# Performance work log

Hardware: AMD Instinct MI355X
Metric: run time of the kernel (lower is better)

## Reference

```python
import jax, jax.numpy as jnp
import numpy as np
import math

B, CIN, COUT, K, R = 8, 128, 128, 7, 2
GC = 16                     # group_channels (init arg `groups`)
G = COUT // GC              # number of dynamic-weight groups = 8
H = W = 32
EPS = 1e-5


def c4_lift(w):
    # w: [o, i, 4] -> dense 1x1 weight [o*4, i*4] via cyclic C4 shifts
    # torch: weight[:, r] = w[..., roll-by-r]  (e.g. r=1 -> [3,0,1,2])
    Wr = jnp.stack([jnp.roll(w, r, axis=-1) for r in range(4)], axis=1)  # [o,4,i,4]
    o, _, i, _ = Wr.shape
    return Wr.reshape(o * 4, i * 4)


def setup_inputs() -> dict:
    key = jax.random.key(0)
    ks = jax.random.split(key, 4)
    sc = 1.0 / math.sqrt(4 * CIN / 2)
    x = jax.random.normal(ks[0], (B, CIN * 4, H, W), dtype=jnp.float32)
    v_w = jax.random.normal(ks[1], (COUT, CIN, 4), dtype=jnp.float32) * sc
    c1_w = jax.random.normal(ks[2], (CIN // R, CIN, 4), dtype=jnp.float32) * sc
    gn_g = jnp.ones((CIN // R * 4,), jnp.float32)
    gn_b = jnp.zeros((CIN // R * 4,), jnp.float32)
    c2_w = jax.random.normal(ks[3], (K * K * G, CIN // R), dtype=jnp.float32) * (1.0 / math.sqrt(CIN // R))
    c2_b = jnp.zeros((K * K * G,), jnp.float32)
    return {"x": x, "v_w": v_w, "c1_w": c1_w, "gn_g": gn_g, "gn_b": gn_b, "c2_w": c2_w, "c2_b": c2_b}


def _forward(x, v_w, c1_w, gn_g, gn_b, c2_w, c2_b):
    b, _, h, w = x.shape
    # conv1: C4-equivariant 1x1
    t = jnp.einsum('oc,bchw->bohw', c4_lift(c1_w), x)        # [b, (CIN//R)*4, h, w]
    # GroupNorm(num_groups=CIN//R) -> normalize each group of 4 channels over (4,h,w)
    tr = t.reshape(b, CIN // R, 4, h, w)
    mu = tr.mean(axis=(2, 3, 4), keepdims=True)
    var = tr.var(axis=(2, 3, 4), keepdims=True)
    t = ((tr - mu) * jax.lax.rsqrt(var + EPS)).reshape(b, CIN // R * 4, h, w)
    t = jax.nn.relu(t * gn_g[None, :, None, None] + gn_b[None, :, None, None])
    # conv2: Conv3d 1x1 over the (c, 4) view
    tv = t.reshape(b, CIN // R, 4, h, w)
    wmap = jnp.einsum('oc,bcrhw->borhw', c2_w, tv) + c2_b[None, :, None, None, None]
    wmap = wmap.reshape(b, G, K, K, 4, h, w)
    # rotate the KxK kernel by r*90deg for C4 element r (r=0 identity)
    wmap = jnp.stack([jnp.rot90(wmap[:, :, :, :, r], k=r, axes=(2, 3)) for r in range(4)], axis=4)
    wmap = wmap.reshape(b, G, K * K, 4, h, w)                 # [b, g, p, r, h, w]
    # v branch (C4 1x1) + unfold (im2col, pad (K-1)//2, stride 1)
    v = jnp.einsum('oc,bchw->bohw', c4_lift(v_w), x)          # [b, COUT*4, h, w]
    p = (K - 1) // 2
    vp = jnp.pad(v, ((0, 0), (0, 0), (p, p), (p, p)))
    patches = jnp.stack([vp[:, :, i:i + h, j:j + w] for i in range(K) for j in range(K)], axis=2)
    patches = patches.reshape(b, G, GC, 4, K * K, h, w)       # [b, g, c, r, p, h, w]
    out = jnp.einsum('bgprhw,bgcrphw->bgcrhw', wmap, patches)
    return out.reshape(b, COUT * 4, h, w)


def reference(x, v_w, c1_w, gn_g, gn_b, c2_w, c2_b):
    return _forward(x, v_w, c1_w, gn_g, gn_b, c2_w, c2_b)
```

## Files before the change

kernel.cpp:

```cpp
#include <hip/hip_runtime.h>

#define BB   8
#define CIN  128
#define COUT 128
#define KS   7
#define HH   32
#define WWID 32
#define HW   1024
#define NG   8
#define GC   16
#define MROWS 768
#define TROWS 256
#define VROWS 512
#define KDIM 512
#define WMAP_O 392
#define WMAP_OP 448
#define C2K  64

typedef __attribute__((ext_vector_type(8))) short bf16x8;
typedef __attribute__((ext_vector_type(4))) float f32x4;

__device__ __forceinline__ short f2bf(float f) {
    unsigned u = __builtin_bit_cast(unsigned, f);
    u += 0x7fff + ((u >> 16) & 1);
    return (short)(u >> 16);
}
__device__ __forceinline__ float bf2f(unsigned short u) {
    unsigned v = (unsigned)u << 16;
    return __builtin_bit_cast(float, v);
}

__global__ __launch_bounds__(256) void prep_kernel(
    const float* __restrict__ x, const float* __restrict__ v_w,
    const float* __restrict__ c1_w, const float* __restrict__ c2_w,
    const float* __restrict__ c2_b,
    short* __restrict__ XT, short* __restrict__ Wb,
    short* __restrict__ c2wb, float* __restrict__ c2bp,
    float* __restrict__ gnstat)
{
    __shared__ short t[64][66];
    int bx = blockIdx.x, tid = threadIdx.x;
    if (bx < 1024) {
        int b = bx >> 7, c0 = ((bx >> 4) & 7) * 64, n0 = (bx & 15) * 64;
        const float* xb = x + ((size_t)b * KDIM + c0) * HW + n0;
        #pragma unroll
        for (int l = 0; l < 16; ++l) {
            int flat = l * 256 + tid;
            int row = flat >> 6, col = flat & 63;
            t[col][row] = f2bf(xb[(size_t)row * HW + col]);
        }
        __syncthreads();
        short* xt = XT + ((size_t)b * HW + n0) * KDIM + c0;
        #pragma unroll
        for (int l = 0; l < 8; ++l) {
            int u = l * 256 + tid;
            int nrow = u >> 5, cp = (u & 31) * 2;
            short2 v = make_short2(t[nrow][cp], t[nrow][cp + 1]);
            *(short2*)(xt + (size_t)nrow * KDIM + cp) = v;
        }
    } else if (bx < 2560) {
        int idx = (bx - 1024) * 256 + tid;
        int row = idx >> 9, col = idx & 511;
        int i = col >> 2, s = col & 3;
        float val;
        if (row < 256) {
            int o = row >> 2, r = row & 3;
            val = c1_w[(o * CIN + i) * 4 + ((s - r) & 3)];
        } else {
            int ro = row - 256;
            int o = ro >> 2, r = ro & 3;
            val = v_w[(o * CIN + i) * 4 + ((s - r) & 3)];
        }
        Wb[idx] = f2bf(val);
    } else if (bx < 2672) {
        int idx = (bx - 2560) * 256 + tid;
        int o = idx >> 6, k = idx & 63;
        c2wb[idx] = f2bf(o < WMAP_O ? c2_w[o * C2K + k] : 0.f);
        if (idx < WMAP_OP)
            c2bp[idx] = idx < WMAP_O ? c2_b[idx] : 0.f;
    } else {
        *(float4*)(gnstat + tid * 4) = make_float4(0.f, 0.f, 0.f, 0.f);
    }
}

#define GBM 64
#define GBN 128
#define GBK 64
__global__ __launch_bounds__(256) void gemm_mfma_kernel(
    const short* __restrict__ Wb, const short* __restrict__ XT,
    short* __restrict__ tvb, float* __restrict__ gnstat)
{
    __shared__ short As[GBM * GBK];
    __shared__ short Bs[GBN * GBK];
    int b  = blockIdx.z;
    int m0 = blockIdx.y * GBM;
    int n0 = blockIdx.x * GBN;
    int tid = threadIdx.x;
    int lane = tid & 63, wv = tid >> 6;
    int wm = wv & 1, wn = wv >> 1;
    int rl = lane & 15, kg = lane >> 4;
    const short* Ab = Wb + (size_t)m0 * KDIM;
    const short* Bb = XT + ((size_t)b * HW + n0) * KDIM;
    f32x4 acc[2][4] = {};

    for (int k0 = 0; k0 < KDIM; k0 += GBK) {
        #pragma unroll
        for (int l = 0; l < 2; ++l) {
            int c = l * 256 + tid;
            int row = c >> 3, kc = c & 7;
            int kcs = kc ^ (row & 7);
            __builtin_amdgcn_global_load_lds(
                (const __attribute__((address_space(1))) void*)(Ab + (size_t)row * KDIM + k0 + kcs * 8),
                (__attribute__((address_space(3))) void*)(As + (l * 256 + wv * 64) * 8),
                16, 0, 0);
        }
        #pragma unroll
        for (int l = 0; l < 4; ++l) {
            int c = l * 256 + tid;
            int row = c >> 3, kc = c & 7;
            int kcs = kc ^ (row & 7);
            __builtin_amdgcn_global_load_lds(
                (const __attribute__((address_space(1))) void*)(Bb + (size_t)row * KDIM + k0 + kcs * 8),
                (__attribute__((address_space(3))) void*)(Bs + (l * 256 + wv * 64) * 8),
                16, 0, 0);
        }
        __syncthreads();
        #pragma unroll
        for (int ks = 0; ks < 2; ++ks) {
            bf16x8 af[2], bfr[4];
            #pragma unroll
            for (int mf = 0; mf < 2; ++mf) {
                int row = wm * 32 + mf * 16 + rl;
                af[mf] = *(const bf16x8*)(As + row * GBK + ((ks * 4 + kg) ^ (row & 7)) * 8);
            }
            #pragma unroll
            for (int nf = 0; nf < 4; ++nf) {
                int row = wn * 64 + nf * 16 + rl;
                bfr[nf] = *(const bf16x8*)(Bs + row * GBK + ((ks * 4 + kg) ^ (row & 7)) * 8);
            }
            #pragma unroll
            for (int mf = 0; mf < 2; ++mf)
                #pragma unroll
                for (int nf = 0; nf < 4; ++nf)
                    acc[mf][nf] = __builtin_amdgcn_mfma_f32_16x16x32_bf16(af[mf], bfr[nf], acc[mf][nf], 0, 0, 0);
        }
        __syncthreads();
    }

    short* Cb = tvb + (size_t)b * MROWS * HW;
    #pragma unroll
    for (int mf = 0; mf < 2; ++mf) {
        int rowb = m0 + wm * 32 + mf * 16 + kg * 4;
        #pragma unroll
        for (int nf = 0; nf < 4; ++nf) {
            int col = n0 + wn * 64 + nf * 16 + rl;
            #pragma unroll
            for (int i = 0; i < 4; ++i)
                Cb[(size_t)(rowb + i) * HW + col] = f2bf(acc[mf][nf][i]);
        }
    }

    if (m0 < TROWS) {
        #pragma unroll
        for (int mf = 0; mf < 2; ++mf) {
            float s = 0.f, sq = 0.f;
            #pragma unroll
            for (int nf = 0; nf < 4; ++nf)
                #pragma unroll
                for (int i = 0; i < 4; ++i) {
                    float v = acc[mf][nf][i];
                    s += v; sq += v * v;
                }
            #pragma unroll
            for (int m = 1; m <= 8; m <<= 1) {
                s  += __shfl_xor(s, m);
                sq += __shfl_xor(sq, m);
            }
            if (rl == 0) {
                int grp = (m0 + wm * 32 + mf * 16 + kg * 4) >> 2;
                atomicAdd(&gnstat[(b * 64 + grp) * 2],     s);
                atomicAdd(&gnstat[(b * 64 + grp) * 2 + 1], sq);
            }
        }
    }
}

__global__ __launch_bounds__(256) void tkn2_kernel(
    const short* __restrict__ tvb, const float* __restrict__ gnstat,
    const float* __restrict__ gn_g, const float* __restrict__ gn_b,
    short* __restrict__ tn)
{
    __shared__ short ts[64][72];
    __shared__ float sc[64], sh[64];
    int b4r = blockIdx.x;
    int b = b4r >> 2, r = b4r & 3;
    int hw0 = blockIdx.y * 64;
    int tid = threadIdx.x;
    if (tid < 64) {
        float s   = gnstat[(b * 64 + tid) * 2];
        float sq  = gnstat[(b * 64 + tid) * 2 + 1];
        float mu  = s * (1.f / 4096.f);
        float var = sq * (1.f / 4096.f) - mu * mu;
        float inv = rsqrtf(var + 1e-5f);
        int ch = tid * 4 + r;
        float g = gn_g[ch], bb = gn_b[ch];
        sc[tid] = inv * g;
        sh[tid] = bb - mu * inv * g;
    }
    #pragma unroll
    for (int l = 0; l < 16; ++l) {
        int flat = l * 256 + tid;
        int c = flat >> 6, hw = flat & 63;
        ts[c][hw] = tvb[((size_t)b * MROWS + c * 4 + r) * HW + hw0 + hw];
    }
    __syncthreads();
    #pragma unroll
    for (int l = 0; l < 2; ++l) {
        int u = l * 256 + tid;
        int hw = u >> 3, c0 = (u & 7) * 8;
        bf16x8 v;
        #pragma unroll
        for (int j = 0; j < 8; ++j) {
            float f = bf2f((unsigned short)ts[c0 + j][hw]);
            f = fmaxf(f * sc[c0 + j] + sh[c0 + j], 0.f);
            v[j] = f2bf(f);
        }
        *(bf16x8*)(tn + ((size_t)b4r * HW + hw0 + hw) * C2K + c0) = v;
    }
}

__global__ __launch_bounds__(256) void wmap3_kernel(
    const short* __restrict__ c2wb, const short* __restrict__ tn,
    const float* __restrict__ c2bp, short* __restrict__ wmapB)
{
    __shared__ short As[64 * 64];
    __shared__ short Bs[128 * 64];
    int n0  = blockIdx.x * 128;
    int m0  = blockIdx.y * 64;
    int b4r = blockIdx.z;
    int tid = threadIdx.x;
    int lane = tid & 63, wv = tid >> 6;
    int wm = wv & 1, wn = wv >> 1;
    int rl = lane & 15, kg = lane >> 4;
    const short* Bb = tn + ((size_t)b4r * HW + n0) * C2K;

    #pragma unroll
    for (int l = 0; l < 2; ++l) {
        int c = l * 256 + tid;
        int row = c >> 3, kc = c & 7;
        int kcs = kc ^ (row & 7);
        __builtin_amdgcn_global_load_lds(
            (const __attribute__((address_space(1))) void*)(c2wb + (size_t)(m0 + row) * C2K + kcs * 8),
            (__attribute__((address_space(3))) void*)(As + (l * 256 + wv * 64) * 8),
            16, 0, 0);
    }
    #pragma unroll
    for (int l = 0; l < 4; ++l) {
        int c = l * 256 + tid;
        int row = c >> 3, kc = c & 7;
        int kcs = kc ^ (row & 7);
        __builtin_amdgcn_global_load_lds(
            (const __attribute__((address_space(1))) void*)(Bb + (size_t)row * C2K + kcs * 8),
            (__attribute__((address_space(3))) void*)(Bs + (l * 256 + wv * 64) * 8),
            16, 0, 0);
    }
    __syncthreads();

    f32x4 acc[2][4] = {};
    #pragma unroll
    for (int ks = 0; ks < 2; ++ks) {
        bf16x8 af[2], bfr[4];
        #pragma unroll
        for (int mf = 0; mf < 2; ++mf) {
            int row = wm * 32 + mf * 16 + rl;
            af[mf] = *(const bf16x8*)(As + row * 64 + ((ks * 4 + kg) ^ (row & 7)) * 8);
        }
        #pragma unroll
        for (int nf = 0; nf < 4; ++nf) {
            int row = wn * 64 + nf * 16 + rl;
            bfr[nf] = *(const bf16x8*)(Bs + row * 64 + ((ks * 4 + kg) ^ (row & 7)) * 8);
        }
        #pragma unroll
        for (int mf = 0; mf < 2; ++mf)
            #pragma unroll
            for (int nf = 0; nf < 4; ++nf)
                acc[mf][nf] = __builtin_amdgcn_mfma_f32_16x16x32_bf16(af[mf], bfr[nf], acc[mf][nf], 0, 0, 0);
    }

    short* wb = wmapB + (size_t)b4r * WMAP_OP * HW;
    #pragma unroll
    for (int mf = 0; mf < 2; ++mf) {
        int rowb = m0 + wm * 32 + mf * 16 + kg * 4;
        float bi[4];
        #pragma unroll
        for (int i = 0; i < 4; ++i) bi[i] = c2bp[rowb + i];
        #pragma unroll
        for (int nf = 0; nf < 4; ++nf) {
            int col = n0 + wn * 64 + nf * 16 + rl;
            #pragma unroll
            for (int i = 0; i < 4; ++i)
                wb[(size_t)(rowb + i) * HW + col] = f2bf(acc[mf][nf][i] + bi[i]);
        }
    }
}

__global__ __launch_bounds__(256, 3) void agg5_kernel(
    const short* __restrict__ tvb, const short* __restrict__ wmapB,
    float* __restrict__ out)
{
    __shared__ float vt[16][15][44];
    int bx = blockIdx.x;
    int b = bx >> 5;
    int g = (bx >> 2) & 7;
    int r = bx & 3;
    int h0  = blockIdx.y * 8;
    int tid = threadIdx.x;
    int w0q = tid & 7, hb = (tid >> 3) & 1, cc4 = (tid >> 4) & 3, cq = tid >> 6;
    int hl = cq * 2 + hb;
    int h = h0 + hl, w0 = w0q * 4;

    int A, Bc, Cc;
    if      (r == 0) { A = 0;  Bc = 7;  Cc = 1;  }
    else if (r == 1) { A = 6;  Bc = -1; Cc = 7;  }
    else if (r == 2) { A = 48; Bc = -7; Cc = -1; }
    else             { A = 42; Bc = 1;  Cc = -7; }

    const short* vpb = tvb + ((size_t)b * MROWS + TROWS) * HW;
    for (int e = tid; e < 16 * 15 * 3; e += 256) {
        int cc  = e / 45;
        int rem = e - cc * 45;
        int row = rem / 3, q = rem - row * 3;
        int col = (q == 0) ? 0 : (36 + (q - 1) * 4);
        *(float4*)(&vt[cc][row][col]) = make_float4(0.f, 0.f, 0.f, 0.f);
    }
    for (int f = tid; f < 16 * 15 * 8; f += 256) {
        int cc  = f / 120;
        int rem = f - cc * 120;
        int row = rem >> 3, q = rem & 7;
        int gh = h0 - 3 + row;
        float4 v4 = make_float4(0.f, 0.f, 0.f, 0.f);
        if (gh >= 0 && gh < HH) {
            int ch = (g * GC + cc) * 4 + r;
            ushort4 u = *(const ushort4*)(vpb + (size_t)ch * HW + gh * WWID + q * 4);
            v4 = make_float4(bf2f(u.x), bf2f(u.y), bf2f(u.z), bf2f(u.w));
        }
        *(float4*)(&vt[cc][row][4 + q * 4]) = v4;
    }
    __syncthreads();

    const short* wmb = wmapB + ((size_t)(b * 4 + r) * WMAP_OP + g * 49) * HW + h * WWID + w0;
    float acc[4][4] = {};
    #pragma unroll
    for (int di = 0; di < 7; ++di) {
        float wrf[7][4];
        #pragma unroll
        for (int dj = 0; dj < 7; ++dj) {
            int porig = A + Bc * di + Cc * dj;
            ushort4 wv = *(const ushort4*)(wmb + (size_t)porig * HW);
            wrf[dj][0] = bf2f(wv.x); wrf[dj][1] = bf2f(wv.y);
            wrf[dj][2] = bf2f(wv.z); wrf[dj][3] = bf2f(wv.w);
        }
        #pragma unroll
        for (int c2 = 0; c2 < 4; ++c2) {
            int hc = cc4 * 4 + c2;
            const float* rp = &vt[hc][hl + di][w0];
            float4 q0 = *(const float4*)(rp);
            float4 q1 = *(const float4*)(rp + 4);
            float4 q2 = *(const float4*)(rp + 8);
            float win[12] = {q0.x, q0.y, q0.z, q0.w,
                             q1.x, q1.y, q1.z, q1.w,
                             q2.x, q2.y, q2.z, q2.w};
            #pragma unroll
            for (int dj = 0; dj < 7; ++dj)
                #pragma unroll
                for (int px = 0; px < 4; ++px)
                    acc[c2][px] += wrf[dj][px] * win[px + dj + 1];
        }
    }
    #pragma unroll
    for (int c2 = 0; c2 < 4; ++c2) {
        int ch = (g * GC + cc4 * 4 + c2) * 4 + r;
        float4 o4 = make_float4(acc[c2][0], acc[c2][1], acc[c2][2], acc[c2][3]);
        *(float4*)(out + ((size_t)b * 512 + ch) * HW + h * WWID + w0) = o4;
    }
}

extern "C" void kernel_launch(void* const* d_in, const int* in_sizes, int n_in,
                              void* d_out, int out_size, void* d_ws, size_t ws_size,
                              hipStream_t stream)
{
    const float* x    = (const float*)d_in[0];
    const float* v_w  = (const float*)d_in[1];
    const float* c1_w = (const float*)d_in[2];
    const float* gn_g = (const float*)d_in[3];
    const float* gn_b = (const float*)d_in[4];
    const float* c2_w = (const float*)d_in[5];
    const float* c2_b = (const float*)d_in[6];
    float* out = (float*)d_out;

    char* p = (char*)d_ws;
    short* Wb     = (short*)p;           p += (size_t)MROWS * KDIM * 2;
    short* tvb    = (short*)p;           p += (size_t)BB * MROWS * HW * 2;
    short* wmapB  = (short*)p;           p += (size_t)32 * WMAP_OP * HW * 2;
    short* XT     = (short*)wmapB;
    short* tn     = (short*)p;           p += (size_t)32 * HW * C2K * 2;
    short* c2wb   = (short*)p;           p += (size_t)WMAP_OP * C2K * 2;
    float* c2bp   = (float*)p;           p += (size_t)WMAP_OP * 4;
    float* gnstat = (float*)p;           p += (size_t)512 * 2 * 4;

    prep_kernel     <<<2673, 256, 0, stream>>>(x, v_w, c1_w, c2_w, c2_b, XT, Wb, c2wb, c2bp, gnstat);
    gemm_mfma_kernel<<<dim3(HW / GBN, MROWS / GBM, BB), 256, 0, stream>>>(Wb, XT, tvb, gnstat);
    tkn2_kernel     <<<dim3(32, 16), 256, 0, stream>>>(tvb, gnstat, gn_g, gn_b, tn);
    wmap3_kernel    <<<dim3(HW / 128, WMAP_OP / 64, 32), 256, 0, stream>>>(c2wb, tn, c2bp, wmapB);
    agg5_kernel     <<<dim3(BB * NG * 4, 4), 256, 0, stream>>>(tvb, wmapB, out);
}
```

Before: 63.17 us.

## Fuse dynamic-weight GEMM into aggregation kernel and double-buffer main GEMM

Merges the wmap GEMM and the aggregation kernel into one kernel. Each block computes its group's 49-tap weight map for 8 rows directly into LDS, which removes the large bf16 wmap round-trip through global memory and one launch. It also double-buffers the LDS tiles in the main C4 GEMM so the next K-slice loads overlap MFMA work. The v-window in LDS is now kept in bf16 to fit the extra weight tile. The costs are heavier LDS use per block, which lowers occupancy, and a dedicated XT workspace that no longer aliases wmap.

```diff
diff --git a/kernel.cpp b/kernel.cpp
--- a/kernel.cpp
+++ b/kernel.cpp
@@ -17,6 +17,9 @@
 #define WMAP_OP 448
 #define C2K  64
 
+#define AS1 __attribute__((address_space(1)))
+#define AS3 __attribute__((address_space(3)))
+
 typedef __attribute__((ext_vector_type(8))) short bf16x8;
 typedef __attribute__((ext_vector_type(4))) float f32x4;
 
@@ -90,8 +93,8 @@
     const short* __restrict__ Wb, const short* __restrict__ XT,
     short* __restrict__ tvb, float* __restrict__ gnstat)
 {
-    __shared__ short As[GBM * GBK];
-    __shared__ short Bs[GBN * GBK];
+    __shared__ short As[2][GBM * GBK];
+    __shared__ short Bs[2][GBN * GBK];
     int b  = blockIdx.z;
     int m0 = blockIdx.y * GBM;
     int n0 = blockIdx.x * GBN;
@@ -103,40 +106,45 @@
     const short* Bb = XT + ((size_t)b * HW + n0) * KDIM;
     f32x4 acc[2][4] = {};
 
-    for (int k0 = 0; k0 < KDIM; k0 += GBK) {
-        #pragma unroll
-        for (int l = 0; l < 2; ++l) {
-            int c = l * 256 + tid;
-            int row = c >> 3, kc = c & 7;
-            int kcs = kc ^ (row & 7);
-            __builtin_amdgcn_global_load_lds(
-                (const __attribute__((address_space(1))) void*)(Ab + (size_t)row * KDIM + k0 + kcs * 8),
-                (__attribute__((address_space(3))) void*)(As + (l * 256 + wv * 64) * 8),
-                16, 0, 0);
-        }
-        #pragma unroll
-        for (int l = 0; l < 4; ++l) {
-            int c = l * 256 + tid;
-            int row = c >> 3, kc = c & 7;
-            int kcs = kc ^ (row & 7);
-            __builtin_amdgcn_global_load_lds(
-                (const __attribute__((address_space(1))) void*)(Bb + (size_t)row * KDIM + k0 + kcs * 8),
-                (__attribute__((address_space(3))) void*)(Bs + (l * 256 + wv * 64) * 8),
-                16, 0, 0);
-        }
-        __syncthreads();
+#define GEMM_STAGE(buf, k0)                                                              \
+    do {                                                                                 \
+        _Pragma("unroll")                                                                \
+        for (int l = 0; l < 2; ++l) {                                                    \
+            int c = l * 256 + tid;                                                       \
+            int row = c >> 3, kc = c & 7;                                                \
+            int kcs = kc ^ (row & 7);                                                    \
+            __builtin_amdgcn_global_load_lds(                                            \
+                (const AS1 void*)(Ab + (size_t)row * KDIM + (k0) + kcs * 8),             \
+                (AS3 void*)(As[buf] + (l * 256 + wv * 64) * 8), 16, 0, 0);               \
+        }                                                                                \
+        _Pragma("unroll")                                                                \
+        for (int l = 0; l < 4; ++l) {                                                    \
+            int c = l * 256 + tid;                                                       \
+            int row = c >> 3, kc = c & 7;                                                \
+            int kcs = kc ^ (row & 7);                                                    \
+            __builtin_amdgcn_global_load_lds(                                            \
+                (const AS1 void*)(Bb + (size_t)row * KDIM + (k0) + kcs * 8),             \
+                (AS3 void*)(Bs[buf] + (l * 256 + wv * 64) * 8), 16, 0, 0);               \
+        }                                                                                \
+    } while (0)
+
+    GEMM_STAGE(0, 0);
+    __syncthreads();
+    for (int t = 0; t < KDIM / GBK; ++t) {
+        int cur = t & 1;
+        if (t < KDIM / GBK - 1) GEMM_STAGE(cur ^ 1, (t + 1) * GBK);
         #pragma unroll
         for (int ks = 0; ks < 2; ++ks) {
             bf16x8 af[2], bfr[4];
             #pragma unroll
             for (int mf = 0; mf < 2; ++mf) {
                 int row = wm * 32 + mf * 16 + rl;
-                af[mf] = *(const bf16x8*)(As + row * GBK + ((ks * 4 + kg) ^ (row & 7)) * 8);
+                af[mf] = *(const bf16x8*)(As[cur] + row * GBK + ((ks * 4 + kg) ^ (row & 7)) * 8);
             }
             #pragma unroll
             for (int nf = 0; nf < 4; ++nf) {
                 int row = wn * 64 + nf * 16 + rl;
-                bfr[nf] = *(const bf16x8*)(Bs + row * GBK + ((ks * 4 + kg) ^ (row & 7)) * 8);
+                bfr[nf] = *(const bf16x8*)(Bs[cur] + row * GBK + ((ks * 4 + kg) ^ (row & 7)) * 8);
             }
             #pragma unroll
             for (int mf = 0; mf < 2; ++mf)
@@ -146,6 +154,7 @@
         }
         __syncthreads();
     }
+#undef GEMM_STAGE
 
     short* Cb = tvb + (size_t)b * MROWS * HW;
     #pragma unroll
@@ -229,20 +238,24 @@
     }
 }
 
-__global__ __launch_bounds__(256) void wmap3_kernel(
+__global__ __launch_bounds__(256) void wagg_kernel(
     const short* __restrict__ c2wb, const short* __restrict__ tn,
-    const float* __restrict__ c2bp, short* __restrict__ wmapB)
+    const float* __restrict__ c2bp, const short* __restrict__ tvb,
+    float* __restrict__ out)
 {
-    __shared__ short As[64 * 64];
-    __shared__ short Bs[128 * 64];
-    int n0  = blockIdx.x * 128;
-    int m0  = blockIdx.y * 64;
-    int b4r = blockIdx.z;
+    __shared__ char smem[62080];
+    short* As_ = (short*)smem;
+    short* Bs_ = (short*)(smem + 8192);
+    short* P   = (short*)smem;
+    unsigned short* vt = (unsigned short*)(smem + 40960);
+
+    int g = blockIdx.x & 7, s = blockIdx.x >> 3;
+    int b4r = blockIdx.y;
+    int b = b4r >> 2, r = b4r & 3;
+    int h0 = s * 8;
     int tid = threadIdx.x;
     int lane = tid & 63, wv = tid >> 6;
-    int wm = wv & 1, wn = wv >> 1;
     int rl = lane & 15, kg = lane >> 4;
-    const short* Bb = tn + ((size_t)b4r * HW + n0) * C2K;
 
     #pragma unroll
     for (int l = 0; l < 2; ++l) {
@@ -250,137 +263,122 @@
         int row = c >> 3, kc = c & 7;
         int kcs = kc ^ (row & 7);
         __builtin_amdgcn_global_load_lds(
-            (const __attribute__((address_space(1))) void*)(c2wb + (size_t)(m0 + row) * C2K + kcs * 8),
-            (__attribute__((address_space(3))) void*)(As + (l * 256 + wv * 64) * 8),
-            16, 0, 0);
-    }
-    #pragma unroll
-    for (int l = 0; l < 4; ++l) {
+            (const AS1 void*)(c2wb + (size_t)(g * 49 + row) * C2K + kcs * 8),
+            (AS3 void*)(As_ + (l * 256 + wv * 64) * 8), 16, 0, 0);
+    }
+    const short* Bb = tn + ((size_t)b4r * HW + s * 256) * C2K;
+    #pragma unroll
+    for (int l = 0; l < 8; ++l) {
         int c = l * 256 + tid;
         int row = c >> 3, kc = c & 7;
         int kcs = kc ^ (row & 7);
         __builtin_amdgcn_global_load_lds(
-            (const __attribute__((address_space(1))) void*)(Bb + (size_t)row * C2K + kcs * 8),
-            (__attribute__((address_space(3))) void*)(Bs + (l * 256 + wv * 64) * 8),
-            16, 0, 0);
+            (const AS1 void*)(Bb + (size_t)row * C2K + kcs * 8),
+            (AS3 void*)(Bs_ + (l * 256 + wv * 64) * 8), 16, 0, 0);
+    }
+    {
+        const short* vpb = tvb + ((size_t)b * MROWS + TROWS) * HW;
+        for (int e = tid; e < 16 * 15 * 3; e += 256) {
+            int cc = e / 45; int rem = e - cc * 45;
+            int row = rem / 3, q = rem - row * 3;
+            int col = (q == 0) ? 0 : (36 + (q - 1) * 4);
+            ushort4 z = {0, 0, 0, 0};
+            *(ushort4*)(&vt[(cc * 15 + row) * 44 + col]) = z;
+        }
+        for (int f = tid; f < 16 * 15 * 8; f += 256) {
+            int cc = f / 120; int rem = f - cc * 120;
+            int row = rem >> 3, q = rem & 7;
+            int gh = h0 - 3 + row;
+            ushort4 u = {0, 0, 0, 0};
+            if (gh >= 0 && gh < HH) {
+                int ch = (g * GC + cc) * 4 + r;
+                u = *(const ushort4*)(vpb + (size_t)ch * HW + gh * WWID + q * 4);
+            }
+            *(ushort4*)(&vt[(cc * 15 + row) * 44 + 4 + q * 4]) = u;
+        }
     }
     __syncthreads();
 
-    f32x4 acc[2][4] = {};
+    f32x4 acc[4][4] = {};
     #pragma unroll
     for (int ks = 0; ks < 2; ++ks) {
-        bf16x8 af[2], bfr[4];
-        #pragma unroll
-        for (int mf = 0; mf < 2; ++mf) {
-            int row = wm * 32 + mf * 16 + rl;
-            af[mf] = *(const bf16x8*)(As + row * 64 + ((ks * 4 + kg) ^ (row & 7)) * 8);
+        bf16x8 af[4], bfr[4];
+        #pragma unroll
+        for (int mf = 0; mf < 4; ++mf) {
+            int row = mf * 16 + rl;
+            af[mf] = *(const bf16x8*)(As_ + row * C2K + ((ks * 4 + kg) ^ (row & 7)) * 8);
         }
         #pragma unroll
         for (int nf = 0; nf < 4; ++nf) {
-            int row = wn * 64 + nf * 16 + rl;
-            bfr[nf] = *(const bf16x8*)(Bs + row * 64 + ((ks * 4 + kg) ^ (row & 7)) * 8);
-        }
-        #pragma unroll
-        for (int mf = 0; mf < 2; ++mf)
+            int row = wv * 64 + nf * 16 + rl;
+            bfr[nf] = *(const bf16x8*)(Bs_ + row * C2K + ((ks * 4 + kg) ^ (row & 7)) * 8);
+        }
+        #pragma unroll
+        for (int mf = 0; mf < 4; ++mf)
             #pragma unroll
             for (int nf = 0; nf < 4; ++nf)
                 acc[mf][nf] = __builtin_amdgcn_mfma_f32_16x16x32_bf16(af[mf], bfr[nf], acc[mf][nf], 0, 0, 0);
     }
-
-    short* wb = wmapB + (size_t)b4r * WMAP_OP * HW;
-    #pragma unroll
-    for (int mf = 0; mf < 2; ++mf) {
-        int rowb = m0 + wm * 32 + mf * 16 + kg * 4;
+    __syncthreads();
+
+    #pragma unroll
+    for (int mf = 0; mf < 4; ++mf) {
+        int rowb = mf * 16 + kg * 4;
         float bi[4];
         #pragma unroll
-        for (int i = 0; i < 4; ++i) bi[i] = c2bp[rowb + i];
+        for (int i = 0; i < 4; ++i) bi[i] = c2bp[g * 49 + rowb + i];
         #pragma unroll
         for (int nf = 0; nf < 4; ++nf) {
-            int col = n0 + wn * 64 + nf * 16 + rl;
+            int col = wv * 64 + nf * 16 + rl;
             #pragma unroll
             for (int i = 0; i < 4; ++i)
-                wb[(size_t)(rowb + i) * HW + col] = f2bf(acc[mf][nf][i] + bi[i]);
-        }
-    }
-}
-
-__global__ __launch_bounds__(256, 3) void agg5_kernel(
-    const short* __restrict__ tvb, const short* __restrict__ wmapB,
-    float* __restrict__ out)
-{
-    __shared__ float vt[16][15][44];
-    int bx = blockIdx.x;
-    int b = bx >> 5;
-    int g = (bx >> 2) & 7;
-    int r = bx & 3;
-    int h0  = blockIdx.y * 8;
-    int tid = threadIdx.x;
+                P[(rowb + i) * 264 + col] = f2bf(acc[mf][nf][i] + bi[i]);
+        }
+    }
+    __syncthreads();
+
     int w0q = tid & 7, hb = (tid >> 3) & 1, cc4 = (tid >> 4) & 3, cq = tid >> 6;
     int hl = cq * 2 + hb;
     int h = h0 + hl, w0 = w0q * 4;
 
-    int A, Bc, Cc;
-    if      (r == 0) { A = 0;  Bc = 7;  Cc = 1;  }
-    else if (r == 1) { A = 6;  Bc = -1; Cc = 7;  }
-    else if (r == 2) { A = 48; Bc = -7; Cc = -1; }
-    else             { A = 42; Bc = 1;  Cc = -7; }
-
-    const short* vpb = tvb + ((size_t)b * MROWS + TROWS) * HW;
-    for (int e = tid; e < 16 * 15 * 3; e += 256) {
-        int cc  = e / 45;
-        int rem = e - cc * 45;
-        int row = rem / 3, q = rem - row * 3;
-        int col = (q == 0) ? 0 : (36 + (q - 1) * 4);
-        *(float4*)(&vt[cc][row][col]) = make_float4(0.f, 0.f, 0.f, 0.f);
-    }
-    for (int f = tid; f < 16 * 15 * 8; f += 256) {
-        int cc  = f / 120;
-        int rem = f - cc * 120;
-        int row = rem >> 3, q = rem & 7;
-        int gh = h0 - 3 + row;
-        float4 v4 = make_float4(0.f, 0.f, 0.f, 0.f);
-        if (gh >= 0 && gh < HH) {
-            int ch = (g * GC + cc) * 4 + r;
-            ushort4 u = *(const ushort4*)(vpb + (size_t)ch * HW + gh * WWID + q * 4);
-            v4 = make_float4(bf2f(u.x), bf2f(u.y), bf2f(u.z), bf2f(u.w));
-        }
-        *(float4*)(&vt[cc][row][4 + q * 4]) = v4;
-    }
-    __syncthreads();
-
-    const short* wmb = wmapB + ((size_t)(b * 4 + r) * WMAP_OP + g * 49) * HW + h * WWID + w0;
-    float acc[4][4] = {};
+    int A_, Bc, Cc;
+    if      (r == 0) { A_ = 0;  Bc = 7;  Cc = 1;  }
+    else if (r == 1) { A_ = 6;  Bc = -1; Cc = 7;  }
+    else if (r == 2) { A_ = 48; Bc = -7; Cc = -1; }
+    else             { A_ = 42; Bc = 1;  Cc = -7; }
+
+    float acc2[4][4] = {};
     #pragma unroll
     for (int di = 0; di < 7; ++di) {
         float wrf[7][4];
         #pragma unroll
         for (int dj = 0; dj < 7; ++dj) {
-            int porig = A + Bc * di + Cc * dj;
-            ushort4 wv = *(const ushort4*)(wmb + (size_t)porig * HW);
-            wrf[dj][0] = bf2f(wv.x); wrf[dj][1] = bf2f(wv.y);
-            wrf[dj][2] = bf2f(wv.z); wrf[dj][3] = bf2f(wv.w);
+            int porig = A_ + Bc * di + Cc * dj;
+            ushort4 wv4 = *(const ushort4*)(&P[porig * 264 + hl * 32 + w0]);
+            wrf[dj][0] = bf2f(wv4.x); wrf[dj][1] = bf2f(wv4.y);
+            wrf[dj][2] = bf2f(wv4.z); wrf[dj][3] = bf2f(wv4.w);
         }
         #pragma unroll
         for (int c2 = 0; c2 < 4; ++c2) {
             int hc = cc4 * 4 + c2;
-            const float* rp = &vt[hc][hl + di][w0];
-            float4 q0 = *(const float4*)(rp);
-            float4 q1 = *(const float4*)(rp + 4);
-            float4 q2 = *(const float4*)(rp + 8);
-            float win[12] = {q0.x, q0.y, q0.z, q0.w,
-                             q1.x, q1.y, q1.z, q1.w,
-                             q2.x, q2.y, q2.z, q2.w};
+            const unsigned short* rp = &vt[(hc * 15 + hl + di) * 44 + w0];
+            ushort4 a0 = *(const ushort4*)(rp);
+            ushort4 a1 = *(const ushort4*)(rp + 4);
+            ushort4 a2 = *(const ushort4*)(rp + 8);
+            float win[12] = {bf2f(a0.x), bf2f(a0.y), bf2f(a0.z), bf2f(a0.w),
+                             bf2f(a1.x), bf2f(a1.y), bf2f(a1.z), bf2f(a1.w),
+                             bf2f(a2.x), bf2f(a2.y), bf2f(a2.z), bf2f(a2.w)};
             #pragma unroll
             for (int dj = 0; dj < 7; ++dj)
                 #pragma unroll
                 for (int px = 0; px < 4; ++px)
-                    acc[c2][px] += wrf[dj][px] * win[px + dj + 1];
+                    acc2[c2][px] += wrf[dj][px] * win[px + dj + 1];
         }
     }
     #pragma unroll
     for (int c2 = 0; c2 < 4; ++c2) {
         int ch = (g * GC + cc4 * 4 + c2) * 4 + r;
-        float4 o4 = make_float4(acc[c2][0], acc[c2][1], acc[c2][2], acc[c2][3]);
+        float4 o4 = make_float4(acc2[c2][0], acc2[c2][1], acc2[c2][2], acc2[c2][3]);
         *(float4*)(out + ((size_t)b * 512 + ch) * HW + h * WWID + w0) = o4;
     }
 }
@@ -401,8 +399,7 @@
     char* p = (char*)d_ws;
     short* Wb     = (short*)p;           p += (size_t)MROWS * KDIM * 2;
     short* tvb    = (short*)p;           p += (size_t)BB * MROWS * HW * 2;
-    short* wmapB  = (short*)p;           p += (size_t)32 * WMAP_OP * HW * 2;
-    short* XT     = (short*)wmapB;
+    short* XT     = (short*)p;           p += (size_t)BB * HW * KDIM * 2;
     short* tn     = (short*)p;           p += (size_t)32 * HW * C2K * 2;
     short* c2wb   = (short*)p;           p += (size_t)WMAP_OP * C2K * 2;
     float* c2bp   = (float*)p;           p += (size_t)WMAP_OP * 4;
@@ -411,6 +408,5 @@
     prep_kernel     <<<2673, 256, 0, stream>>>(x, v_w, c1_w, c2_w, c2_b, XT, Wb, c2wb, c2bp, gnstat);
     gemm_mfma_kernel<<<dim3(HW / GBN, MROWS / GBM, BB), 256, 0, stream>>>(Wb, XT, tvb, gnstat);
     tkn2_kernel     <<<dim3(32, 16), 256, 0, stream>>>(tvb, gnstat, gn_g, gn_b, tn);
-    wmap3_kernel    <<<dim3(HW / 128, WMAP_OP / 64, 32), 256, 0, stream>>>(c2wb, tn, c2bp, wmapB);
-    agg5_kernel     <<<dim3(BB * NG * 4, 4), 256, 0, stream>>>(tvb, wmapB, out);
-}
+    wagg_kernel     <<<dim3(32, 32), 256, 0, stream>>>(c2wb, tn, c2bp, tvb, out);
+}
```

Result: slower. 85.46 us (+35.3%).

## Stage wmap GEMM output through LDS and shrink aggregation tiles

Applied to the files above, without the earlier changes.

The wmap GEMM epilogue now writes its bf16 results into shared memory first, then stores them to global memory as coalesced 16-byte row segments and skips the padded rows beyond 392. This replaces the scattered 2-byte stores. The aggregation kernel now covers 4 output rows per block instead of 8, with 2 channels per thread instead of 4. That doubles the grid, cuts LDS and register use so the launch bound can ask for 5 blocks per CU, and costs more halo reloading of the v tile and more wmap loads per output.

```diff
diff --git a/kernel.cpp b/kernel.cpp
--- a/kernel.cpp
+++ b/kernel.cpp
@@ -17,6 +17,9 @@
 #define WMAP_OP 448
 #define C2K  64
 
+#define AS1 __attribute__((address_space(1)))
+#define AS3 __attribute__((address_space(3)))
+
 typedef __attribute__((ext_vector_type(8))) short bf16x8;
 typedef __attribute__((ext_vector_type(4))) float f32x4;
 
@@ -110,9 +113,8 @@
             int row = c >> 3, kc = c & 7;
             int kcs = kc ^ (row & 7);
             __builtin_amdgcn_global_load_lds(
-                (const __attribute__((address_space(1))) void*)(Ab + (size_t)row * KDIM + k0 + kcs * 8),
-                (__attribute__((address_space(3))) void*)(As + (l * 256 + wv * 64) * 8),
-                16, 0, 0);
+                (const AS1 void*)(Ab + (size_t)row * KDIM + k0 + kcs * 8),
+                (AS3 void*)(As + (l * 256 + wv * 64) * 8), 16, 0, 0);
         }
         #pragma unroll
         for (int l = 0; l < 4; ++l) {
@@ -120,9 +122,8 @@
             int row = c >> 3, kc = c & 7;
             int kcs = kc ^ (row & 7);
             __builtin_amdgcn_global_load_lds(
-                (const __attribute__((address_space(1))) void*)(Bb + (size_t)row * KDIM + k0 + kcs * 8),
-                (__attribute__((address_space(3))) void*)(Bs + (l * 256 + wv * 64) * 8),
-                16, 0, 0);
+                (const AS1 void*)(Bb + (size_t)row * KDIM + k0 + kcs * 8),
+                (AS3 void*)(Bs + (l * 256 + wv * 64) * 8), 16, 0, 0);
         }
         __syncthreads();
         #pragma unroll
@@ -233,8 +234,10 @@
     const short* __restrict__ c2wb, const short* __restrict__ tn,
     const float* __restrict__ c2bp, short* __restrict__ wmapB)
 {
-    __shared__ short As[64 * 64];
-    __shared__ short Bs[128 * 64];
+    __shared__ short smem[64 * 64 + 128 * 64];
+    short* As = smem;
+    short* Bs = smem + 64 * 64;
+    short* Ps = smem;
     int n0  = blockIdx.x * 128;
     int m0  = blockIdx.y * 64;
     int b4r = blockIdx.z;
@@ -250,9 +253,8 @@
         int row = c >> 3, kc = c & 7;
         int kcs = kc ^ (row & 7);
         __builtin_amdgcn_global_load_lds(
-            (const __attribute__((address_space(1))) void*)(c2wb + (size_t)(m0 + row) * C2K + kcs * 8),
-            (__attribute__((address_space(3))) void*)(As + (l * 256 + wv * 64) * 8),
-            16, 0, 0);
+            (const AS1 void*)(c2wb + (size_t)(m0 + row) * C2K + kcs * 8),
+            (AS3 void*)(As + (l * 256 + wv * 64) * 8), 16, 0, 0);
     }
     #pragma unroll
     for (int l = 0; l < 4; ++l) {
@@ -260,9 +262,8 @@
         int row = c >> 3, kc = c & 7;
         int kcs = kc ^ (row & 7);
         __builtin_amdgcn_global_load_lds(
-            (const __attribute__((address_space(1))) void*)(Bb + (size_t)row * C2K + kcs * 8),
-            (__attribute__((address_space(3))) void*)(Bs + (l * 256 + wv * 64) * 8),
-            16, 0, 0);
+            (const AS1 void*)(Bb + (size_t)row * C2K + kcs * 8),
+            (AS3 void*)(Bs + (l * 256 + wv * 64) * 8), 16, 0, 0);
     }
     __syncthreads();
 
@@ -286,37 +287,47 @@
             for (int nf = 0; nf < 4; ++nf)
                 acc[mf][nf] = __builtin_amdgcn_mfma_f32_16x16x32_bf16(af[mf], bfr[nf], acc[mf][nf], 0, 0, 0);
     }
-
-    short* wb = wmapB + (size_t)b4r * WMAP_OP * HW;
+    __syncthreads();
+
     #pragma unroll
     for (int mf = 0; mf < 2; ++mf) {
-        int rowb = m0 + wm * 32 + mf * 16 + kg * 4;
+        int rowl = wm * 32 + mf * 16 + kg * 4;
         float bi[4];
         #pragma unroll
-        for (int i = 0; i < 4; ++i) bi[i] = c2bp[rowb + i];
+        for (int i = 0; i < 4; ++i) bi[i] = c2bp[m0 + rowl + i];
         #pragma unroll
         for (int nf = 0; nf < 4; ++nf) {
-            int col = n0 + wn * 64 + nf * 16 + rl;
+            int col = wn * 64 + nf * 16 + rl;
             #pragma unroll
             for (int i = 0; i < 4; ++i)
-                wb[(size_t)(rowb + i) * HW + col] = f2bf(acc[mf][nf][i] + bi[i]);
-        }
-    }
-}
-
-__global__ __launch_bounds__(256, 3) void agg5_kernel(
+                Ps[(rowl + i) * 136 + col] = f2bf(acc[mf][nf][i] + bi[i]);
+        }
+    }
+    __syncthreads();
+
+    int row = tid >> 2, segl = tid & 3;
+    if (m0 + row < WMAP_O) {
+        short* dst = wmapB + (size_t)b4r * WMAP_OP * HW + (size_t)(m0 + row) * HW + n0;
+        #pragma unroll
+        for (int s2 = 0; s2 < 4; ++s2) {
+            int col = segl * 8 + s2 * 32;
+            *(bf16x8*)(dst + col) = *(const bf16x8*)(Ps + row * 136 + col);
+        }
+    }
+}
+
+__global__ __launch_bounds__(256, 5) void agg7_kernel(
     const short* __restrict__ tvb, const short* __restrict__ wmapB,
     float* __restrict__ out)
 {
-    __shared__ float vt[16][15][44];
+    __shared__ float vt[16][10][44];
     int bx = blockIdx.x;
     int b = bx >> 5;
     int g = (bx >> 2) & 7;
     int r = bx & 3;
-    int h0  = blockIdx.y * 8;
+    int h0  = blockIdx.y * 4;
     int tid = threadIdx.x;
-    int w0q = tid & 7, hb = (tid >> 3) & 1, cc4 = (tid >> 4) & 3, cq = tid >> 6;
-    int hl = cq * 2 + hb;
+    int w0q = tid & 7, hl = (tid >> 3) & 3, cp = tid >> 5;
     int h = h0 + hl, w0 = w0q * 4;
 
     int A, Bc, Cc;
@@ -326,16 +337,16 @@
     else             { A = 42; Bc = 1;  Cc = -7; }
 
     const short* vpb = tvb + ((size_t)b * MROWS + TROWS) * HW;
-    for (int e = tid; e < 16 * 15 * 3; e += 256) {
-        int cc  = e / 45;
-        int rem = e - cc * 45;
+    for (int e = tid; e < 480; e += 256) {
+        int cc  = e / 30;
+        int rem = e - cc * 30;
         int row = rem / 3, q = rem - row * 3;
         int col = (q == 0) ? 0 : (36 + (q - 1) * 4);
         *(float4*)(&vt[cc][row][col]) = make_float4(0.f, 0.f, 0.f, 0.f);
     }
-    for (int f = tid; f < 16 * 15 * 8; f += 256) {
-        int cc  = f / 120;
-        int rem = f - cc * 120;
+    for (int f = tid; f < 1280; f += 256) {
+        int cc  = f / 80;
+        int rem = f - cc * 80;
         int row = rem >> 3, q = rem & 7;
         int gh = h0 - 3 + row;
         float4 v4 = make_float4(0.f, 0.f, 0.f, 0.f);
@@ -349,7 +360,7 @@
     __syncthreads();
 
     const short* wmb = wmapB + ((size_t)(b * 4 + r) * WMAP_OP + g * 49) * HW + h * WWID + w0;
-    float acc[4][4] = {};
+    float acc[2][4] = {};
     #pragma unroll
     for (int di = 0; di < 7; ++di) {
         float wrf[7][4];
@@ -361,8 +372,8 @@
             wrf[dj][2] = bf2f(wv.z); wrf[dj][3] = bf2f(wv.w);
         }
         #pragma unroll
-        for (int c2 = 0; c2 < 4; ++c2) {
-            int hc = cc4 * 4 + c2;
+        for (int c2 = 0; c2 < 2; ++c2) {
+            int hc = cp * 2 + c2;
             const float* rp = &vt[hc][hl + di][w0];
             float4 q0 = *(const float4*)(rp);
             float4 q1 = *(const float4*)(rp + 4);
@@ -378,8 +389,8 @@
         }
     }
     #pragma unroll
-    for (int c2 = 0; c2 < 4; ++c2) {
-        int ch = (g * GC + cc4 * 4 + c2) * 4 + r;
+    for (int c2 = 0; c2 < 2; ++c2) {
+        int ch = (g * GC + cp * 2 + c2) * 4 + r;
         float4 o4 = make_float4(acc[c2][0], acc[c2][1], acc[c2][2], acc[c2][3]);
         *(float4*)(out + ((size_t)b * 512 + ch) * HW + h * WWID + w0) = o4;
     }
@@ -412,5 +423,5 @@
     gemm_mfma_kernel<<<dim3(HW / GBN, MROWS / GBM, BB), 256, 0, stream>>>(Wb, XT, tvb, gnstat);
     tkn2_kernel     <<<dim3(32, 16), 256, 0, stream>>>(tvb, gnstat, gn_g, gn_b, tn);
     wmap3_kernel    <<<dim3(HW / 128, WMAP_OP / 64, 32), 256, 0, stream>>>(c2wb, tn, c2bp, wmapB);
-    agg5_kernel     <<<dim3(BB * NG * 4, 4), 256, 0, stream>>>(tvb, wmapB, out);
-}
+    agg7_kernel     <<<dim3(BB * NG * 4, 8), 256, 0, stream>>>(tvb, wmapB, out);
+}
```

Measured after the change: 62.68 us. About the same (-0.8%).
